# Optimization experiments

Measured on AMD Instinct MI355X. Metric: run time of the kernel, lower is better.

The kernel has to match this reference:

```python
import jax, jax.numpy as jnp
import numpy as np

B, N, D, H, DH = 4, 4096, 1024, 8, 64
INNER = H * DH
EPS = 1e-5


def setup_inputs() -> dict:
    key = jax.random.key(0)
    ks = jax.random.split(key, 8)
    x = jax.random.normal(ks[0], (B, N, D), dtype=jnp.float32)
    W_qkv = jax.random.normal(ks[1], (3 * INNER, D), dtype=jnp.float32) * 0.02
    gamma_q = 1.0 + 0.1 * jax.random.normal(ks[2], (H, DH), dtype=jnp.float32)
    beta_q = 0.1 * jax.random.normal(ks[3], (H, DH), dtype=jnp.float32)
    gamma_k = 1.0 + 0.1 * jax.random.normal(ks[4], (H, DH), dtype=jnp.float32)
    beta_k = 0.1 * jax.random.normal(ks[5], (H, DH), dtype=jnp.float32)
    W_out = jax.random.normal(ks[6], (D, INNER), dtype=jnp.float32) * 0.02
    b_out = jnp.zeros((D,), dtype=jnp.float32)
    return {"x": x, "W_qkv": W_qkv, "gamma_q": gamma_q, "beta_q": beta_q,
            "gamma_k": gamma_k, "beta_k": beta_k, "W_out": W_out, "b_out": b_out}


def _per_head_layernorm(t, gamma, beta):
    # t: [B, H, N, DH]; gamma/beta: [H, DH] (one LayerNorm per head)
    m = jnp.mean(t, axis=-1, keepdims=True)
    var = jnp.mean(jnp.square(t - m), axis=-1, keepdims=True)
    tn = (t - m) * jax.lax.rsqrt(var + EPS)
    return tn * gamma[None, :, None, :] + beta[None, :, None, :]


def reference(x, W_qkv, gamma_q, beta_q, gamma_k, beta_k, W_out, b_out):
    b, n, d = x.shape
    h, dh = gamma_q.shape
    qkv = x @ W_qkv.T                                   # [B, N, 3*H*DH]
    q, k, v = jnp.split(qkv, 3, axis=-1)
    to_heads = lambda t: t.reshape(b, n, h, dh).transpose(0, 2, 1, 3)  # [B,H,N,DH]
    q, k, v = to_heads(q), to_heads(k), to_heads(v)
    q = _per_head_layernorm(q, gamma_q, beta_q)
    k = _per_head_layernorm(k, gamma_k, beta_k)
    # Softmax-free Galerkin attention: (Q K^T V) / (sqrt(dh) * n) reassociated
    # as Q (K^T V) -- mathematically identical, linear in n.
    scale = 1.0 / (jnp.sqrt(jnp.asarray(dh, x.dtype)) * n)
    kv = jnp.einsum('bhnd,bhne->bhde', k, v)            # [B,H,DH,DH]
    out = jnp.einsum('bhnd,bhde->bhne', q, kv) * scale  # [B,H,N,DH]
    out = out.transpose(0, 2, 1, 3).reshape(b, n, h * dh)
    return out @ W_out.T + b_out
```

## Files before the change

kernel.cpp:

```cpp
#include <hip/hip_runtime.h>
#include <stdint.h>

typedef unsigned short u16;
typedef unsigned int u32;
typedef __bf16 bf16x8 __attribute__((ext_vector_type(8)));
typedef float f32x4 __attribute__((ext_vector_type(4)));

__device__ __forceinline__ float bf2f(u16 u) {
  return __builtin_bit_cast(float, (u32)u << 16);
}
__device__ __forceinline__ u16 f2b(float f) {
  u32 u = __builtin_bit_cast(u32, f);
  u32 r = (u + 0x7fffu + ((u >> 16) & 1u)) >> 16;
  return (u16)r;
}
__device__ __forceinline__ void gload16(const u16* g, u16* l) {
  __builtin_amdgcn_global_load_lds(
      (const __attribute__((address_space(1))) u32*)(const void*)g,
      (__attribute__((address_space(3))) u32*)(void*)l, 16, 0, 0);
}
__device__ __forceinline__ void unpack16(uint4 a, uint4 b, float* o) {
  u32 w[8] = {a.x, a.y, a.z, a.w, b.x, b.y, b.z, b.w};
#pragma unroll
  for (int i = 0; i < 8; ++i) {
    o[2 * i]     = __builtin_bit_cast(float, w[i] << 16);
    o[2 * i + 1] = __builtin_bit_cast(float, w[i] & 0xffff0000u);
  }
}

__global__ __launch_bounds__(256) void cvt3(
    const float* __restrict__ a, u16* __restrict__ ao, int na4,
    const float* __restrict__ b, u16* __restrict__ bo, int nb4,
    const float* __restrict__ c, u16* __restrict__ co, int nc4) {
  const int total = na4 + nb4 + nc4;
  for (int i = blockIdx.x * 256 + threadIdx.x; i < total; i += gridDim.x * 256) {
    const float4* src;
    ushort4* dst;
    int idx;
    if (i < na4) {
      src = reinterpret_cast<const float4*>(a); dst = reinterpret_cast<ushort4*>(ao); idx = i;
    } else if (i < na4 + nb4) {
      src = reinterpret_cast<const float4*>(b); dst = reinterpret_cast<ushort4*>(bo); idx = i - na4;
    } else {
      src = reinterpret_cast<const float4*>(c); dst = reinterpret_cast<ushort4*>(co); idx = i - na4 - nb4;
    }
    float4 v = src[idx];
    ushort4 o;
    o.x = f2b(v.x); o.y = f2b(v.y); o.z = f2b(v.z); o.w = f2b(v.w);
    dst[idx] = o;
  }
}

template <int MODE, int TB>
__global__ __launch_bounds__(256, (TB == 3) ? 3 : 4) void gemm_bt(
    const u16* __restrict__ A, const u16* __restrict__ B, void* __restrict__ C,
    const float* __restrict__ gq, const float* __restrict__ bq,
    const float* __restrict__ gk, const float* __restrict__ bk,
    const float* __restrict__ bias, int M, int N, int K, int ntn,
    int lda, size_t bstride) {
  __shared__ u16 As[TB][128 * 32];
  __shared__ u16 Bs[TB][128 * 32];

  const int nwg = gridDim.x;
  const int bid0 = blockIdx.x;
  const int bid = (bid0 & 7) * (nwg >> 3) + (bid0 >> 3);
  const int tm = bid / ntn, tn = bid % ntn;
  const int brow = tm << 7, bcol = tn << 7;
  const int tid = threadIdx.x;
  const int w = tid >> 6, lane = tid & 63;
  const int wrow = (w >> 1) << 6, wcol = (w & 1) << 6;
  const int lr = lane & 15, lg = lane >> 4;

  const u16* Bp = (MODE == 1) ? (B + (size_t)(brow >> 12) * bstride) : B;

  const int sslot = (lane & 3) ^ ((lane >> 3) & 3);
  const u16* Asrc = A + (size_t)(brow + (lane >> 2)) * lda + sslot * 8;
  const u16* Bsrc = Bp + (size_t)(bcol + (lane >> 2)) * K + sslot * 8;

  auto stage = [&](int t, int buf) {
    const int k0 = t << 5;
#pragma unroll
    for (int i = 0; i < 2; ++i) {
      int g = w + 4 * i;
      gload16(Asrc + (size_t)(16 * g) * lda + k0, &As[buf][(16 * g) * 32]);
      gload16(Bsrc + (size_t)(16 * g) * K + k0, &Bs[buf][(16 * g) * 32]);
    }
  };

  f32x4 acc[4][4];
#pragma unroll
  for (int m = 0; m < 4; ++m)
#pragma unroll
    for (int n = 0; n < 4; ++n) acc[m][n] = (f32x4){0.f, 0.f, 0.f, 0.f};

  const int NC = K >> 5;
  const int kslot = (lg ^ ((lr >> 1) & 3)) << 3;

  auto compute = [&](const u16* Asb, const u16* Bsb) {
    bf16x8 af[4], bfr[4];
#pragma unroll
    for (int m = 0; m < 4; ++m)
      af[m] = *reinterpret_cast<const bf16x8*>(&Asb[(wrow + m * 16 + lr) * 32 + kslot]);
#pragma unroll
    for (int n = 0; n < 4; ++n)
      bfr[n] = *reinterpret_cast<const bf16x8*>(&Bsb[(wcol + n * 16 + lr) * 32 + kslot]);
    __builtin_amdgcn_s_setprio(1);
#pragma unroll
    for (int m = 0; m < 4; ++m)
#pragma unroll
      for (int n = 0; n < 4; ++n)
        acc[m][n] = __builtin_amdgcn_mfma_f32_16x16x32_bf16(af[m], bfr[n], acc[m][n], 0, 0, 0);
    __builtin_amdgcn_s_setprio(0);
  };

  if constexpr (TB == 3) {
    stage(0, 0);
    stage(1, 1);
    int cur = 0, nx2 = 2;
    for (int t = 0; t < NC; ++t) {
      if (t + 1 < NC)
        asm volatile("s_waitcnt vmcnt(4)" ::: "memory");
      else
        asm volatile("s_waitcnt vmcnt(0)" ::: "memory");
      __builtin_amdgcn_s_barrier();
      asm volatile("" ::: "memory");
      if (t + 2 < NC) stage(t + 2, nx2);
      compute(As[cur], Bs[cur]);
      asm volatile("" ::: "memory");
      cur = (cur == 2) ? 0 : cur + 1;
      nx2 = (nx2 == 2) ? 0 : nx2 + 1;
    }
  } else {
    stage(0, 0);
    __syncthreads();
    for (int t = 0; t < NC; ++t) {
      const int cur = t & 1;
      if (t + 1 < NC) stage(t + 1, cur ^ 1);
      compute(As[cur], Bs[cur]);
      __syncthreads();
    }
  }

  const int orow = brow + wrow + ((lane >> 4) << 2);
  const int ocol = bcol + wcol + lr;
  if (MODE == 0) {
    const int wcol0 = bcol + wcol;
    const int sect = wcol0 >> 6;
    const bool doln = sect < 16;
    const float* Gp = (sect < 8) ? (gq + wcol0) : (gk + (wcol0 - 512));
    const float* Pp = (sect < 8) ? (bq + wcol0) : (bk + (wcol0 - 512));
    float gv[4], pv[4];
    if (doln) {
#pragma unroll
      for (int n = 0; n < 4; ++n) { gv[n] = Gp[n * 16 + lr]; pv[n] = Pp[n * 16 + lr]; }
    }
    u16* Cp = (u16*)C;
#pragma unroll
    for (int m = 0; m < 4; ++m)
#pragma unroll
      for (int r = 0; r < 4; ++r) {
        size_t rowoff = (size_t)(orow + m * 16 + r) * N;
        if (doln) {
          float s = 0.f, s2 = 0.f;
#pragma unroll
          for (int n = 0; n < 4; ++n) {
            float x = acc[m][n][r];
            s += x; s2 += x * x;
          }
#pragma unroll
          for (int off = 8; off; off >>= 1) {
            s += __shfl_xor(s, off, 64);
            s2 += __shfl_xor(s2, off, 64);
          }
          float mean = s * 0.015625f;
          float inv = rsqrtf(s2 * 0.015625f - mean * mean + 1e-5f);
#pragma unroll
          for (int n = 0; n < 4; ++n)
            Cp[rowoff + ocol + n * 16] =
                f2b((acc[m][n][r] - mean) * inv * gv[n] + pv[n]);
        } else {
#pragma unroll
          for (int n = 0; n < 4; ++n)
            Cp[rowoff + ocol + n * 16] = f2b(acc[m][n][r]);
        }
      }
  } else {
    float bvv[4];
#pragma unroll
    for (int n = 0; n < 4; ++n) bvv[n] = bias[ocol + n * 16];
    float* Cp = (float*)C;
#pragma unroll
    for (int m = 0; m < 4; ++m)
#pragma unroll
      for (int r = 0; r < 4; ++r) {
        size_t rowoff = (size_t)(orow + m * 16 + r) * N;
#pragma unroll
        for (int n = 0; n < 4; ++n)
          Cp[rowoff + ocol + n * 16] = acc[m][n][r] + bvv[n];
      }
  }
}

__global__ __launch_bounds__(256) void kv_accum(const u16* __restrict__ qkv,
                                                float* __restrict__ KVpart) {
  int nch = blockIdx.x & 15;
  int bh = blockIdx.x >> 4;
  int b = bh >> 3, h = bh & 7;
  __shared__ float ks[64][64];
  __shared__ float vs[64][64];
  int tid = threadIdx.x;
  int ty = tid >> 4, tx = tid & 15;
  int rr = tid >> 2, cc = (tid & 3) * 16;
  float acc[4][4];
#pragma unroll
  for (int i = 0; i < 4; ++i)
#pragma unroll
    for (int j = 0; j < 4; ++j) acc[i][j] = 0.f;

  for (int t = 0; t < 4; ++t) {
    int n0 = nch * 256 + t * 64;
    __syncthreads();
    size_t base = ((size_t)(b * 4096 + n0 + rr)) * 1536 + h * 64 + cc;
    const uint4* kp = reinterpret_cast<const uint4*>(&qkv[base + 512]);
    const uint4* vp = reinterpret_cast<const uint4*>(&qkv[base + 1024]);
    uint4 k0 = kp[0], k1 = kp[1];
    uint4 v0 = vp[0], v1 = vp[1];
    unpack16(k0, k1, &ks[rr][cc]);
    unpack16(v0, v1, &vs[rr][cc]);
    __syncthreads();
    for (int n = 0; n < 64; ++n) {
      float4 k4 = *reinterpret_cast<const float4*>(&ks[n][ty * 4]);
      float4 v4 = *reinterpret_cast<const float4*>(&vs[n][tx * 4]);
      float ka[4] = {k4.x, k4.y, k4.z, k4.w};
      float va[4] = {v4.x, v4.y, v4.z, v4.w};
#pragma unroll
      for (int i = 0; i < 4; ++i)
#pragma unroll
        for (int j = 0; j < 4; ++j) acc[i][j] += ka[i] * va[j];
    }
  }
  float* dst = KVpart + ((size_t)(bh * 16 + nch)) * 4096;
#pragma unroll
  for (int i = 0; i < 4; ++i) {
    float4 st = {acc[i][0], acc[i][1], acc[i][2], acc[i][3]};
    *reinterpret_cast<float4*>(&dst[(ty * 4 + i) * 64 + tx * 4]) = st;
  }
}

__global__ __launch_bounds__(256) void kv_reduce(const float* __restrict__ KVpart,
                                                 float* __restrict__ KV) {
  int bh = blockIdx.x;
  int t = threadIdx.x;
  const float4* src = reinterpret_cast<const float4*>(KVpart + (size_t)bh * 16 * 4096);
  float4* dst = reinterpret_cast<float4*>(KV + (size_t)bh * 4096);
#pragma unroll
  for (int i = 0; i < 4; ++i) {
    int idx = t + 256 * i;
    float4 s = src[idx];
#pragma unroll
    for (int c = 1; c < 16; ++c) {
      float4 v = src[c * 1024 + idx];
      s.x += v.x; s.y += v.y; s.z += v.z; s.w += v.w;
    }
    dst[idx] = s;
  }
}

__global__ __launch_bounds__(256) void w2_kernel(const float* __restrict__ KV,
                                                 const u16* __restrict__ wob,
                                                 u16* __restrict__ w2) {
  int bh = blockIdx.x & 31, jt = blockIdx.x >> 5;
  int b = bh >> 3, h = bh & 7;
  __shared__ float kvs[64][64];
  int t = threadIdx.x;
  {
    const float4* src = reinterpret_cast<const float4*>(KV + (size_t)bh * 4096);
    float4* dst = reinterpret_cast<float4*>(&kvs[0][0]);
#pragma unroll
    for (int i = 0; i < 4; ++i) dst[t + 256 * i] = src[t + 256 * i];
  }
  __syncthreads();
  int jloc = t & 127, dg = t >> 7;
  int j = jt * 128 + jloc;
  float wo[64];
  const u16* wr = wob + (size_t)j * 512 + h * 64;
#pragma unroll
  for (int e8 = 0; e8 < 8; ++e8) {
    uint4 pk = *reinterpret_cast<const uint4*>(wr + e8 * 8);
    u32 wds[4] = {pk.x, pk.y, pk.z, pk.w};
#pragma unroll
    for (int i = 0; i < 4; ++i) {
      wo[e8 * 8 + 2 * i]     = bf2f((u16)(wds[i] & 0xffffu));
      wo[e8 * 8 + 2 * i + 1] = bf2f((u16)(wds[i] >> 16));
    }
  }
  const float scale = 1.0f / 32768.0f;
  u16* outp = w2 + ((size_t)b * 1024 + j) * 512 + h * 64 + dg * 32;
#pragma unroll
  for (int dd = 0; dd < 32; ++dd) {
    int d = dg * 32 + dd;
    float acc = 0.f;
    const float4* kr = reinterpret_cast<const float4*>(&kvs[d][0]);
#pragma unroll
    for (int e4 = 0; e4 < 16; ++e4) {
      float4 kv4 = kr[e4];
      acc += kv4.x * wo[e4 * 4] + kv4.y * wo[e4 * 4 + 1] +
             kv4.z * wo[e4 * 4 + 2] + kv4.w * wo[e4 * 4 + 3];
    }
    outp[dd] = f2b(acc * scale);
  }
}

extern "C" void kernel_launch(void* const* d_in, const int* in_sizes, int n_in,
                              void* d_out, int out_size, void* d_ws, size_t ws_size,
                              hipStream_t stream) {
  const float* x  = (const float*)d_in[0];
  const float* Wq = (const float*)d_in[1];
  const float* gq = (const float*)d_in[2];
  const float* bq = (const float*)d_in[3];
  const float* gk = (const float*)d_in[4];
  const float* bk = (const float*)d_in[5];
  const float* Wo = (const float*)d_in[6];
  const float* bo = (const float*)d_in[7];
  float* out = (float*)d_out;

  char* p = (char*)d_ws;
  auto carve = [&](size_t bytes) {
    char* r = p;
    p += (bytes + 255) & ~(size_t)255;
    return r;
  };
  u16* xb      = (u16*)carve((size_t)16384 * 1024 * 2);
  u16* wqb     = (u16*)carve((size_t)1536 * 1024 * 2);
  u16* wob     = (u16*)carve((size_t)1024 * 512 * 2);
  u16* qkv     = (u16*)carve((size_t)16384 * 1536 * 2);
  float* KVp   = (float*)carve((size_t)32 * 16 * 4096 * 4);
  float* KVb   = (float*)carve((size_t)32 * 4096 * 4);
  u16* w2b     = (u16*)carve((size_t)4 * 1024 * 512 * 2);

  cvt3<<<2048, 256, 0, stream>>>(x, xb, 4194304, Wq, wqb, 393216, Wo, wob, 131072);
  gemm_bt<0, 3><<<128 * 12, 256, 0, stream>>>(xb, wqb, qkv, gq, bq, gk, bk,
                                              nullptr, 16384, 1536, 1024, 12,
                                              1024, 0);
  kv_accum<<<512, 256, 0, stream>>>(qkv, KVp);
  kv_reduce<<<32, 256, 0, stream>>>(KVp, KVb);
  w2_kernel<<<256, 256, 0, stream>>>(KVb, wob, w2b);
  gemm_bt<1, 2><<<128 * 8, 256, 0, stream>>>(qkv, w2b, out, nullptr, nullptr,
                                             nullptr, nullptr, bo, 16384, 1024,
                                             512, 8, 1536, (size_t)1024 * 512);
}
```

Measured before the change: 155.4 us.

## Load QKV GEMM B operand directly into registers, stage only A in LDS

Splits the templated GEMM into a QKV kernel and an output kernel. The QKV kernel no longer stages the weight tile in LDS. Each wave loads its B fragments straight from global memory into registers, double-buffered across a manually unrolled-by-two loop, while A stays in a triple-buffered LDS ring. This halves LDS footprint and traffic and raises the occupancy hint from 3 to 4. In exchange the per-wave B loads are less coalesced and each wave re-fetches weight data that was previously shared through LDS.

```diff
diff --git a/kernel.cpp b/kernel.cpp
--- a/kernel.cpp
+++ b/kernel.cpp
@@ -51,15 +51,13 @@
   }
 }
 
-template <int MODE, int TB>
-__global__ __launch_bounds__(256, (TB == 3) ? 3 : 4) void gemm_bt(
-    const u16* __restrict__ A, const u16* __restrict__ B, void* __restrict__ C,
+template <int KK>
+__global__ __launch_bounds__(256, 4) void gemm_qkv(
+    const u16* __restrict__ A, const u16* __restrict__ B, u16* __restrict__ C,
     const float* __restrict__ gq, const float* __restrict__ bq,
     const float* __restrict__ gk, const float* __restrict__ bk,
-    const float* __restrict__ bias, int M, int N, int K, int ntn,
-    int lda, size_t bstride) {
-  __shared__ u16 As[TB][128 * 32];
-  __shared__ u16 Bs[TB][128 * 32];
+    int N, int ntn) {
+  __shared__ u16 As[3][128 * 32];
 
   const int nwg = gridDim.x;
   const int bid0 = blockIdx.x;
@@ -71,7 +69,136 @@
   const int wrow = (w >> 1) << 6, wcol = (w & 1) << 6;
   const int lr = lane & 15, lg = lane >> 4;
 
-  const u16* Bp = (MODE == 1) ? (B + (size_t)(brow >> 12) * bstride) : B;
+  const int sslot = (lane & 3) ^ ((lane >> 3) & 3);
+  const u16* Asrc = A + (size_t)(brow + (lane >> 2)) * KK + sslot * 8;
+  auto stageA = [&](int t, int buf) {
+    const int k0 = t << 5;
+#pragma unroll
+    for (int i = 0; i < 2; ++i) {
+      int g = w + 4 * i;
+      gload16(Asrc + (size_t)(16 * g) * KK + k0, &As[buf][(16 * g) * 32]);
+    }
+  };
+
+  const u16* Bg = B + (size_t)(bcol + wcol + lr) * KK + lg * 8;
+  auto loadB = [&](int t, uint4 (&br)[4]) {
+#pragma unroll
+    for (int n = 0; n < 4; ++n)
+      br[n] = *reinterpret_cast<const uint4*>(Bg + (size_t)(n * 16) * KK + (t << 5));
+  };
+
+  f32x4 acc[4][4];
+#pragma unroll
+  for (int m = 0; m < 4; ++m)
+#pragma unroll
+    for (int n = 0; n < 4; ++n) acc[m][n] = (f32x4){0.f, 0.f, 0.f, 0.f};
+
+  constexpr int NC = KK >> 5;
+  const int kslot = (lg ^ ((lr >> 1) & 3)) << 3;
+
+  uint4 brA[4], brB[4];
+  loadB(0, brA);
+  stageA(0, 0);
+  stageA(1, 1);
+
+  auto body = [&](int t, int cur3, int nx3, uint4(&brCur)[4], uint4(&brNxt)[4]) {
+    if (t + 1 < NC)
+      asm volatile("s_waitcnt vmcnt(2)" ::: "memory");
+    else
+      asm volatile("s_waitcnt vmcnt(0)" ::: "memory");
+    __builtin_amdgcn_s_barrier();
+    asm volatile("" ::: "memory");
+    if (t + 1 < NC) loadB(t + 1, brNxt);
+    if (t + 2 < NC) stageA(t + 2, nx3);
+
+    const u16* Asb = As[cur3];
+    bf16x8 af[4], bfr[4];
+#pragma unroll
+    for (int m = 0; m < 4; ++m)
+      af[m] = *reinterpret_cast<const bf16x8*>(&Asb[(wrow + m * 16 + lr) * 32 + kslot]);
+#pragma unroll
+    for (int n = 0; n < 4; ++n) bfr[n] = __builtin_bit_cast(bf16x8, brCur[n]);
+    __builtin_amdgcn_s_setprio(1);
+#pragma unroll
+    for (int m = 0; m < 4; ++m)
+#pragma unroll
+      for (int n = 0; n < 4; ++n)
+        acc[m][n] = __builtin_amdgcn_mfma_f32_16x16x32_bf16(af[m], bfr[n], acc[m][n], 0, 0, 0);
+    __builtin_amdgcn_s_setprio(0);
+    asm volatile("" ::: "memory");
+  };
+
+  int c3 = 0, n3 = 2;
+  for (int tt = 0; tt < NC; tt += 2) {
+    body(tt, c3, n3, brA, brB);
+    c3 = (c3 == 2) ? 0 : c3 + 1;
+    n3 = (n3 == 2) ? 0 : n3 + 1;
+    body(tt + 1, c3, n3, brB, brA);
+    c3 = (c3 == 2) ? 0 : c3 + 1;
+    n3 = (n3 == 2) ? 0 : n3 + 1;
+  }
+
+  const int orow = brow + wrow + ((lane >> 4) << 2);
+  const int ocol = bcol + wcol + lr;
+  const int wcol0 = bcol + wcol;
+  const int sect = wcol0 >> 6;
+  const bool doln = sect < 16;
+  const float* Gp = (sect < 8) ? (gq + wcol0) : (gk + (wcol0 - 512));
+  const float* Pp = (sect < 8) ? (bq + wcol0) : (bk + (wcol0 - 512));
+  float gv[4], pv[4];
+  if (doln) {
+#pragma unroll
+    for (int n = 0; n < 4; ++n) { gv[n] = Gp[n * 16 + lr]; pv[n] = Pp[n * 16 + lr]; }
+  }
+#pragma unroll
+  for (int m = 0; m < 4; ++m)
+#pragma unroll
+    for (int r = 0; r < 4; ++r) {
+      size_t rowoff = (size_t)(orow + m * 16 + r) * N;
+      if (doln) {
+        float s = 0.f, s2 = 0.f;
+#pragma unroll
+        for (int n = 0; n < 4; ++n) {
+          float x = acc[m][n][r];
+          s += x; s2 += x * x;
+        }
+#pragma unroll
+        for (int off = 8; off; off >>= 1) {
+          s += __shfl_xor(s, off, 64);
+          s2 += __shfl_xor(s2, off, 64);
+        }
+        float mean = s * 0.015625f;
+        float inv = rsqrtf(s2 * 0.015625f - mean * mean + 1e-5f);
+#pragma unroll
+        for (int n = 0; n < 4; ++n)
+          C[rowoff + ocol + n * 16] =
+              f2b((acc[m][n][r] - mean) * inv * gv[n] + pv[n]);
+      } else {
+#pragma unroll
+        for (int n = 0; n < 4; ++n)
+          C[rowoff + ocol + n * 16] = f2b(acc[m][n][r]);
+      }
+    }
+}
+
+__global__ __launch_bounds__(256, 4) void gemm_out(
+    const u16* __restrict__ A, const u16* __restrict__ B, float* __restrict__ C,
+    const float* __restrict__ bias, int M, int N, int K, int ntn,
+    int lda, size_t bstride) {
+  __shared__ u16 As[2][128 * 32];
+  __shared__ u16 Bs[2][128 * 32];
+
+  const int nwg = gridDim.x;
+  const int bid0 = blockIdx.x;
+  const int bid = (bid0 & 7) * (nwg >> 3) + (bid0 >> 3);
+  const int tm = bid / ntn, tn = bid % ntn;
+  const int brow = tm << 7, bcol = tn << 7;
+  const int tid = threadIdx.x;
+  const int w = tid >> 6, lane = tid & 63;
+  const int wrow = (w >> 1) << 6, wcol = (w & 1) << 6;
+  const int lr = lane & 15, lg = lane >> 4;
+
+  const u16* Bp = B + (size_t)(brow >> 12) * bstride;
 
   const int sslot = (lane & 3) ^ ((lane >> 3) & 3);
   const u16* Asrc = A + (size_t)(brow + (lane >> 2)) * lda + sslot * 8;
@@ -96,7 +223,13 @@
   const int NC = K >> 5;
   const int kslot = (lg ^ ((lr >> 1) & 3)) << 3;
 
-  auto compute = [&](const u16* Asb, const u16* Bsb) {
+  stage(0, 0);
+  __syncthreads();
+  for (int t = 0; t < NC; ++t) {
+    const int cur = t & 1;
+    if (t + 1 < NC) stage(t + 1, cur ^ 1);
+    const u16* Asb = As[cur];
+    const u16* Bsb = Bs[cur];
     bf16x8 af[4], bfr[4];
 #pragma unroll
     for (int m = 0; m < 4; ++m)
@@ -111,94 +244,23 @@
       for (int n = 0; n < 4; ++n)
         acc[m][n] = __builtin_amdgcn_mfma_f32_16x16x32_bf16(af[m], bfr[n], acc[m][n], 0, 0, 0);
     __builtin_amdgcn_s_setprio(0);
-  };
-
-  if constexpr (TB == 3) {
-    stage(0, 0);
-    stage(1, 1);
-    int cur = 0, nx2 = 2;
-    for (int t = 0; t < NC; ++t) {
-      if (t + 1 < NC)
-        asm volatile("s_waitcnt vmcnt(4)" ::: "memory");
-      else
-        asm volatile("s_waitcnt vmcnt(0)" ::: "memory");
-      __builtin_amdgcn_s_barrier();
-      asm volatile("" ::: "memory");
-      if (t + 2 < NC) stage(t + 2, nx2);
-      compute(As[cur], Bs[cur]);
-      asm volatile("" ::: "memory");
-      cur = (cur == 2) ? 0 : cur + 1;
-      nx2 = (nx2 == 2) ? 0 : nx2 + 1;
-    }
-  } else {
-    stage(0, 0);
     __syncthreads();
-    for (int t = 0; t < NC; ++t) {
-      const int cur = t & 1;
-      if (t + 1 < NC) stage(t + 1, cur ^ 1);
-      compute(As[cur], Bs[cur]);
-      __syncthreads();
-    }
   }
 
   const int orow = brow + wrow + ((lane >> 4) << 2);
   const int ocol = bcol + wcol + lr;
-  if (MODE == 0) {
-    const int wcol0 = bcol + wcol;
-    const int sect = wcol0 >> 6;
-    const bool doln = sect < 16;
-    const float* Gp = (sect < 8) ? (gq + wcol0) : (gk + (wcol0 - 512));
-    const float* Pp = (sect < 8) ? (bq + wcol0) : (bk + (wcol0 - 512));
-    float gv[4], pv[4];
-    if (doln) {
-#pragma unroll
-      for (int n = 0; n < 4; ++n) { gv[n] = Gp[n * 16 + lr]; pv[n] = Pp[n * 16 + lr]; }
-    }
-    u16* Cp = (u16*)C;
-#pragma unroll
-    for (int m = 0; m < 4; ++m)
-#pragma unroll
-      for (int r = 0; r < 4; ++r) {
-        size_t rowoff = (size_t)(orow + m * 16 + r) * N;
-        if (doln) {
-          float s = 0.f, s2 = 0.f;
-#pragma unroll
-          for (int n = 0; n < 4; ++n) {
-            float x = acc[m][n][r];
-            s += x; s2 += x * x;
-          }
-#pragma unroll
-          for (int off = 8; off; off >>= 1) {
-            s += __shfl_xor(s, off, 64);
-            s2 += __shfl_xor(s2, off, 64);
-          }
-          float mean = s * 0.015625f;
-          float inv = rsqrtf(s2 * 0.015625f - mean * mean + 1e-5f);
-#pragma unroll
-          for (int n = 0; n < 4; ++n)
-            Cp[rowoff + ocol + n * 16] =
-                f2b((acc[m][n][r] - mean) * inv * gv[n] + pv[n]);
-        } else {
-#pragma unroll
-          for (int n = 0; n < 4; ++n)
-            Cp[rowoff + ocol + n * 16] = f2b(acc[m][n][r]);
-        }
-      }
-  } else {
-    float bvv[4];
-#pragma unroll
-    for (int n = 0; n < 4; ++n) bvv[n] = bias[ocol + n * 16];
-    float* Cp = (float*)C;
-#pragma unroll
-    for (int m = 0; m < 4; ++m)
-#pragma unroll
-      for (int r = 0; r < 4; ++r) {
-        size_t rowoff = (size_t)(orow + m * 16 + r) * N;
-#pragma unroll
-        for (int n = 0; n < 4; ++n)
-          Cp[rowoff + ocol + n * 16] = acc[m][n][r] + bvv[n];
-      }
-  }
+  float bvv[4];
+#pragma unroll
+  for (int n = 0; n < 4; ++n) bvv[n] = bias[ocol + n * 16];
+#pragma unroll
+  for (int m = 0; m < 4; ++m)
+#pragma unroll
+    for (int r = 0; r < 4; ++r) {
+      size_t rowoff = (size_t)(orow + m * 16 + r) * N;
+#pragma unroll
+      for (int n = 0; n < 4; ++n)
+        C[rowoff + ocol + n * 16] = acc[m][n][r] + bvv[n];
+    }
 }
 
 __global__ __launch_bounds__(256) void kv_accum(const u16* __restrict__ qkv,
@@ -339,13 +401,11 @@
   u16* w2b     = (u16*)carve((size_t)4 * 1024 * 512 * 2);
 
   cvt3<<<2048, 256, 0, stream>>>(x, xb, 4194304, Wq, wqb, 393216, Wo, wob, 131072);
-  gemm_bt<0, 3><<<128 * 12, 256, 0, stream>>>(xb, wqb, qkv, gq, bq, gk, bk,
-                                              nullptr, 16384, 1536, 1024, 12,
-                                              1024, 0);
+  gemm_qkv<1024><<<128 * 12, 256, 0, stream>>>(xb, wqb, qkv, gq, bq, gk, bk,
+                                               1536, 12);
   kv_accum<<<512, 256, 0, stream>>>(qkv, KVp);
   kv_reduce<<<32, 256, 0, stream>>>(KVp, KVb);
   w2_kernel<<<256, 256, 0, stream>>>(KVb, wob, w2b);
-  gemm_bt<1, 2><<<128 * 8, 256, 0, stream>>>(qkv, w2b, out, nullptr, nullptr,
-                                             nullptr, nullptr, bo, 16384, 1024,
-                                             512, 8, 1536, (size_t)1024 * 512);
-}
+  gemm_out<<<128 * 8, 256, 0, stream>>>(qkv, w2b, out, bo, 16384, 1024, 512, 8,
+                                        1536, (size_t)1024 * 512);
+}
```

New measurement: 198.0 us. +27.4%, slower.
